# Kernel optimization log

Measured on AMD Instinct MI355X. Metric: run time of the kernel, lower is better.

The kernel has to match this reference:

```python
import jax, jax.numpy as jnp
import numpy as np

B, T, F = 2048, 128, 1
H1, H2 = 128, 64


def lstm_relu(x, W, U, b):
    """Keras LSTM with activation=relu, recurrent_activation=sigmoid.
    x: [B, T, Fin]; W: [Fin, 4H]; U: [H, 4H]; b: [4H]. Gate order i,f,g,o.
    Returns full sequence of hidden states [B, T, H]."""
    Bb = x.shape[0]
    H = U.shape[0]

    def step(carry, xt):
        h, c = carry
        z = xt @ W + h @ U + b  # [B, 4H]
        i, f, g, o = jnp.split(z, 4, axis=-1)
        i = jax.nn.sigmoid(i)
        f = jax.nn.sigmoid(f)
        o = jax.nn.sigmoid(o)
        g = jax.nn.relu(g)
        c = f * c + i * g
        h = o * jax.nn.relu(c)
        return (h, c), h

    h0 = jnp.zeros((Bb, H), x.dtype)
    (_, _), hs = jax.lax.scan(step, (h0, h0), jnp.swapaxes(x, 0, 1))
    return jnp.swapaxes(hs, 0, 1)  # [B, T, H]


def setup_inputs() -> dict:
    key = jax.random.key(0)
    ks = jax.random.split(key, 16)
    s = 0.05  # small init so relu LSTM stays numerically stable
    d = {
        "x": jax.random.normal(ks[0], (B, T, F), jnp.float32),
        "W1": jax.random.normal(ks[1], (F, 4 * H1), jnp.float32) * s,
        "U1": jax.random.normal(ks[2], (H1, 4 * H1), jnp.float32) * s,
        "b1": jnp.zeros((4 * H1,), jnp.float32),
        "W2": jax.random.normal(ks[3], (H1, 4 * H2), jnp.float32) * s,
        "U2": jax.random.normal(ks[4], (H2, 4 * H2), jnp.float32) * s,
        "b2": jnp.zeros((4 * H2,), jnp.float32),
        "W3": jax.random.normal(ks[5], (H2, 4 * H2), jnp.float32) * s,
        "U3": jax.random.normal(ks[6], (H2, 4 * H2), jnp.float32) * s,
        "b3": jnp.zeros((4 * H2,), jnp.float32),
        "W4": jax.random.normal(ks[7], (H2, 4 * H1), jnp.float32) * s,
        "U4": jax.random.normal(ks[8], (H1, 4 * H1), jnp.float32) * s,
        "b4": jnp.zeros((4 * H1,), jnp.float32),
        "Wd": jax.random.normal(ks[9], (H1, 1), jnp.float32) * s,
        "bd": jnp.zeros((1,), jnp.float32),
    }
    return d


def reference(x, W1, U1, b1, W2, U2, b2, W3, U3, b3, W4, U4, b4, Wd, bd):
    h = lstm_relu(x, W1, U1, b1)            # [B, T, 128]
    h = lstm_relu(h, W2, U2, b2)[:, -1]     # return_sequences=False -> [B, 64]
    h = jnp.broadcast_to(h[:, None, :], (h.shape[0], T, h.shape[-1]))  # RepeatVector
    h = lstm_relu(h, W3, U3, b3)            # [B, T, 64]
    h = lstm_relu(h, W4, U4, b4)            # [B, T, 128]
    out = h @ Wd + bd                       # TimeDistributed Dense(1) -> [B, T, 1]
    return out
```

## Files before the change

kernel.cpp:

```cpp
#include <hip/hip_runtime.h>


#define TSEQ 128
#define NTH  512
#define BSTR 408

typedef __attribute__((ext_vector_type(8))) short bf16x8;
typedef __attribute__((ext_vector_type(4))) float f32x4;
typedef __attribute__((ext_vector_type(2))) float f32x2;
typedef __attribute__((ext_vector_type(4))) short s16x4;
typedef unsigned short ushort_t;

#define FB_L1 0
#define FB_L2 256
#define FB_L3 448
#define FB_L4 512
#define FB_W3 896
#define WS_FRAGS 960
#define WS_NEEDED (WS_FRAGS * 1024)

__device__ __forceinline__ ushort_t f2bf(float f) {
    union { float f; unsigned u; } a; a.f = f;
    unsigned r = a.u + 0x7FFF + ((a.u >> 16) & 1);
    return (ushort_t)(r >> 16);
}
__device__ __forceinline__ float bf2f(ushort_t h) {
    union { unsigned u; float f; } a; a.u = ((unsigned)h) << 16;
    return a.f;
}
__device__ __forceinline__ float sigm(float z) { return 1.0f / (1.0f + __expf(-z)); }

__device__ __forceinline__ f32x4 MF(bf16x8 a, bf16x8 b, f32x4 c) {
    return __builtin_amdgcn_mfma_f32_16x16x32_bf16(a, b, c, 0, 0, 0);
}

__global__ void pack_weights(const float* __restrict__ U1, const float* __restrict__ W2,
                             const float* __restrict__ U2, const float* __restrict__ U3,
                             const float* __restrict__ W4, const float* __restrict__ U4,
                             const float* __restrict__ W3, ushort_t* __restrict__ out)
{
    const int f = blockIdx.x;
    const int lane = threadIdx.x;
    int fl, KT, ldm, ksplit = 1 << 30, ld2 = 0;
    const float *base, *base2 = nullptr;
    if (f < 256)      { fl = f;       KT = 4; ldm = 512; base = U1; }
    else if (f < 448) { fl = f - 256; KT = 6; ldm = 256; base = W2; ksplit = 128; base2 = U2; ld2 = 256; }
    else if (f < 512) { fl = f - 448; KT = 2; ldm = 256; base = U3; }
    else if (f < 896) { fl = f - 512; KT = 6; ldm = 512; base = W4; ksplit = 64;  base2 = U4; ld2 = 512; }
    else              { fl = f - 896; KT = 2; ldm = 256; base = W3; }
    const int jt = fl / (KT * 2);
    const int rem = fl % (KT * 2);
    const int kt = rem >> 1;
    const int s = rem & 1;
    const int j = jt * 16 + (lane & 15);
    ushort_t* o = out + f * 512 + lane * 8;
    #pragma unroll
    for (int i = 0; i < 8; ++i) {
        const int k = kt * 32 + (lane >> 4) * 8 + i;
        const float w = (k < ksplit) ? base[k * ldm + j] : base2[(k - ksplit) * ld2 + j];
        const ushort_t hi = f2bf(w);
        o[i] = s ? f2bf(w - bf2f(hi)) : hi;
    }
}

__global__ __launch_bounds__(NTH, 2) void lstm_mfma_kernel(
    const float* __restrict__ x,
    const float* __restrict__ W1, const float* __restrict__ b1,
    const float* __restrict__ b2, const float* __restrict__ b3,
    const float* __restrict__ b4,
    const float* __restrict__ Wd, const float* __restrict__ bd,
    const ushort_t* __restrict__ wsp,
    float* __restrict__ out)
{
    __shared__ __align__(16) ushort_t bU[16][BSTR];
    __shared__ __align__(16) float zb[16][260];
    __shared__ __align__(16) float z3x[16][260];
    __shared__ __align__(16) float c23[16][64];
    __shared__ __align__(16) float obuf[16][128];
    __shared__ __align__(16) float xls[16][132];
    __shared__ __align__(16) float w1ls[512], b1ls[512], b4ls[512], b2ls[256];

    const int tid  = threadIdx.x;
    const int wid  = tid >> 6;
    const int lane = tid & 63;
    const int quad = lane >> 4;
    const int l15  = lane & 15;
    const int r0   = blockIdx.x * 16;
    const bf16x8* A = (const bf16x8*)wsp;

    const int rg = tid >> 5;
    const int jp = (tid & 31) * 2;

    {
        unsigned* p = (unsigned*)&bU[0][0];
        for (int i = tid; i < 16 * BSTR / 2; i += NTH) p[i] = 0u;
        float* q = &c23[0][0];
        for (int i = tid; i < 16 * 64; i += NTH) q[i] = 0.f;
        const int srow = tid >> 5, scol = (tid & 31) * 4;
        *(f32x4*)&xls[srow][scol] = *(const f32x4*)&x[(r0 + srow) * TSEQ + scol];
        w1ls[tid] = W1[tid];
        b1ls[tid] = b1[tid];
        b4ls[tid] = b4[tid];
        if (tid < 256) b2ls[tid] = b2[tid];
    }

    const int hcb = 16 * wid + quad * 4;
    const float wd0 = Wd[lane], wd1 = Wd[64 + lane], bd0 = bd[0];

    float c1r[4] = {0.f, 0.f, 0.f, 0.f};
    float c4r[4] = {0.f, 0.f, 0.f, 0.f};

    __syncthreads();

    {
        bf16x8 wL1[16], wL2[12];
        #pragma unroll
        for (int q = 0; q < 4; ++q)
            #pragma unroll
            for (int kt = 0; kt < 4; ++kt)
                wL1[q * 4 + kt] = A[(FB_L1 + ((wid + 8 * q) * 4 + kt) * 2) * 64 + lane];
        #pragma unroll
        for (int jj = 0; jj < 2; ++jj)
            #pragma unroll
            for (int kt = 0; kt < 6; ++kt)
                wL2[jj * 6 + kt] = A[(FB_L2 + ((2 * wid + jj) * 6 + kt) * 2) * 64 + lane];

        for (int t = 0; t < TSEQ; ++t) {
            const int rb1 = (t & 1) * 128, wb1 = 128 - rb1;

            {
                bf16x8 Bh[4];
                #pragma unroll
                for (int kt = 0; kt < 4; ++kt)
                    Bh[kt] = *(const bf16x8*)&bU[l15][rb1 + kt * 32 + quad * 8];
                const float xr = xls[l15][t];
                f32x4 acc[4];
                #pragma unroll
                for (int q = 0; q < 4; ++q) {
                    const int jb = (wid + 8 * q) * 16 + quad * 4;
                    f32x4 a = *(const f32x4*)&b1ls[jb];
                    a += xr * *(const f32x4*)&w1ls[jb];
                    #pragma unroll
                    for (int kt = 0; kt < 4; ++kt)
                        a = MF(wL1[q * 4 + kt], Bh[kt], a);
                    acc[q] = a;
                }
                s16x4 hv;
                #pragma unroll
                for (int g = 0; g < 4; ++g) {
                    const float zi = acc[0][g];
                    const float zf = acc[1][g];
                    const float zg = acc[2][g];
                    const float zo = acc[3][g];
                    const float c = sigm(zf) * c1r[g] + sigm(zi) * fmaxf(zg, 0.f);
                    c1r[g] = c;
                    const float h = sigm(zo) * fmaxf(c, 0.f);
                    hv[g] = (short)f2bf(h);
                }
                *(s16x4*)&bU[l15][wb1 + hcb] = hv;
            }
            __syncthreads();

            {
                bf16x8 Bh[6];
                #pragma unroll
                for (int kt = 0; kt < 4; ++kt)
                    Bh[kt] = *(const bf16x8*)&bU[l15][wb1 + kt * 32 + quad * 8];
                #pragma unroll
                for (int kt = 4; kt < 6; ++kt)
                    Bh[kt] = *(const bf16x8*)&bU[l15][256 + (kt - 4) * 32 + quad * 8];
                #pragma unroll
                for (int jj = 0; jj < 2; ++jj) {
                    const int jt = 2 * wid + jj;
                    f32x4 a = *(const f32x4*)&b2ls[jt * 16 + quad * 4];
                    #pragma unroll
                    for (int kt = 0; kt < 6; ++kt)
                        a = MF(wL2[jj * 6 + kt], Bh[kt], a);
                    *(f32x4*)&zb[l15][jt * 16 + quad * 4] = a;
                }
            }
            __syncthreads();

            {
                const f32x2 zi = *(const f32x2*)&zb[rg][jp];
                const f32x2 zf = *(const f32x2*)&zb[rg][64 + jp];
                const f32x2 zg = *(const f32x2*)&zb[rg][128 + jp];
                const f32x2 zo = *(const f32x2*)&zb[rg][192 + jp];
                f32x2 c = *(const f32x2*)&c23[rg][jp];
                unsigned hw = 0;
                #pragma unroll
                for (int k = 0; k < 2; ++k) {
                    const float cc = sigm(zf[k]) * c[k] + sigm(zi[k]) * fmaxf(zg[k], 0.f);
                    c[k] = cc;
                    const float h = sigm(zo[k]) * fmaxf(cc, 0.f);
                    hw |= ((unsigned)f2bf(h)) << (16 * k);
                }
                *(f32x2*)&c23[rg][jp] = c;
                *(unsigned*)&bU[rg][256 + jp] = hw;
            }
        }
    }
    __syncthreads();

    {
        bf16x8 Bh[2];
        #pragma unroll
        for (int kt = 0; kt < 2; ++kt)
            Bh[kt] = *(const bf16x8*)&bU[l15][256 + kt * 32 + quad * 8];
        #pragma unroll
        for (int jj = 0; jj < 2; ++jj) {
            const int jt = 2 * wid + jj;
            f32x4 a = *(const f32x4*)&b3[jt * 16 + quad * 4];
            #pragma unroll
            for (int kt = 0; kt < 2; ++kt) {
                const bf16x8 ah = A[(FB_W3 + (jt * 2 + kt) * 2) * 64 + lane];
                a = MF(ah, Bh[kt], a);
            }
            *(f32x4*)&z3x[l15][jt * 16 + quad * 4] = a;
        }
    }
    __syncthreads();
    {
        unsigned* p = (unsigned*)&bU[0][0];
        for (int i = tid; i < 16 * BSTR / 2; i += NTH) p[i] = 0u;
        float* q = &c23[0][0];
        for (int i = tid; i < 16 * 64; i += NTH) q[i] = 0.f;
        c4r[0] = c4r[1] = c4r[2] = c4r[3] = 0.f;
    }
    __syncthreads();

    {
        bf16x8 wL3[4], wL4[24];
        #pragma unroll
        for (int jj = 0; jj < 2; ++jj)
            #pragma unroll
            for (int kt = 0; kt < 2; ++kt)
                wL3[jj * 2 + kt] = A[(FB_L3 + ((2 * wid + jj) * 2 + kt) * 2) * 64 + lane];
        #pragma unroll
        for (int q = 0; q < 4; ++q)
            #pragma unroll
            for (int kt = 0; kt < 6; ++kt)
                wL4[q * 6 + kt] = A[(FB_L4 + ((wid + 8 * q) * 6 + kt) * 2) * 64 + lane];

        for (int t = 0; t < TSEQ; ++t) {
            const int rb3 = (t & 1) * 64, wb3 = 64 - rb3;
            const int rb4 = 128 + (t & 1) * 128;
            const int wb4 = (rb4 == 128) ? 256 : 128;

            {
                bf16x8 Bh[2];
                #pragma unroll
                for (int kt = 0; kt < 2; ++kt)
                    Bh[kt] = *(const bf16x8*)&bU[l15][rb3 + kt * 32 + quad * 8];
                #pragma unroll
                for (int jj = 0; jj < 2; ++jj) {
                    const int jt = 2 * wid + jj;
                    f32x4 a = {0.f, 0.f, 0.f, 0.f};
                    #pragma unroll
                    for (int kt = 0; kt < 2; ++kt)
                        a = MF(wL3[jj * 2 + kt], Bh[kt], a);
                    *(f32x4*)&zb[l15][jt * 16 + quad * 4] = a;
                }
            }
            __syncthreads();

            {
                const f32x2 zi = *(const f32x2*)&zb[rg][jp]       + *(const f32x2*)&z3x[rg][jp];
                const f32x2 zf = *(const f32x2*)&zb[rg][64 + jp]  + *(const f32x2*)&z3x[rg][64 + jp];
                const f32x2 zg = *(const f32x2*)&zb[rg][128 + jp] + *(const f32x2*)&z3x[rg][128 + jp];
                const f32x2 zo = *(const f32x2*)&zb[rg][192 + jp] + *(const f32x2*)&z3x[rg][192 + jp];
                f32x2 c = *(const f32x2*)&c23[rg][jp];
                unsigned hw = 0;
                #pragma unroll
                for (int k = 0; k < 2; ++k) {
                    const float cc = sigm(zf[k]) * c[k] + sigm(zi[k]) * fmaxf(zg[k], 0.f);
                    c[k] = cc;
                    const float h = sigm(zo[k]) * fmaxf(cc, 0.f);
                    hw |= ((unsigned)f2bf(h)) << (16 * k);
                }
                *(f32x2*)&c23[rg][jp] = c;
                *(unsigned*)&bU[rg][wb3 + jp] = hw;

                if (t > 0) {
                    #pragma unroll
                    for (int e = 0; e < 2; ++e) {
                        const int r = wid + 8 * e;
                        const float h0 = bf2f(bU[r][rb4 + lane]);
                        const float h1_ = bf2f(bU[r][rb4 + 64 + lane]);
                        float v = h0 * wd0 + h1_ * wd1;
                        v += __shfl_down(v, 32);
                        v += __shfl_down(v, 16);
                        v += __shfl_down(v, 8);
                        v += __shfl_down(v, 4);
                        v += __shfl_down(v, 2);
                        v += __shfl_down(v, 1);
                        if (lane == 0) obuf[r][t - 1] = v + bd0;
                    }
                }
            }
            __syncthreads();

            {
                bf16x8 Bh[6];
                #pragma unroll
                for (int kt = 0; kt < 2; ++kt)
                    Bh[kt] = *(const bf16x8*)&bU[l15][wb3 + kt * 32 + quad * 8];
                #pragma unroll
                for (int kt = 2; kt < 6; ++kt)
                    Bh[kt] = *(const bf16x8*)&bU[l15][rb4 + (kt - 2) * 32 + quad * 8];
                f32x4 acc[4];
                #pragma unroll
                for (int q = 0; q < 4; ++q) {
                    f32x4 a = *(const f32x4*)&b4ls[(wid + 8 * q) * 16 + quad * 4];
                    #pragma unroll
                    for (int kt = 0; kt < 6; ++kt)
                        a = MF(wL4[q * 6 + kt], Bh[kt], a);
                    acc[q] = a;
                }
                s16x4 hv;
                #pragma unroll
                for (int g = 0; g < 4; ++g) {
                    const float zi = acc[0][g];
                    const float zf = acc[1][g];
                    const float zg = acc[2][g];
                    const float zo = acc[3][g];
                    const float c = sigm(zf) * c4r[g] + sigm(zi) * fmaxf(zg, 0.f);
                    c4r[g] = c;
                    const float h = sigm(zo) * fmaxf(c, 0.f);
                    hv[g] = (short)f2bf(h);
                }
                *(s16x4*)&bU[l15][wb4 + hcb] = hv;
            }
        }
    }
    __syncthreads();
    {
        #pragma unroll
        for (int e = 0; e < 2; ++e) {
            const int r = wid + 8 * e;
            const float h0 = bf2f(bU[r][128 + lane]);
            const float h1_ = bf2f(bU[r][128 + 64 + lane]);
            float v = h0 * wd0 + h1_ * wd1;
            v += __shfl_down(v, 32);
            v += __shfl_down(v, 16);
            v += __shfl_down(v, 8);
            v += __shfl_down(v, 4);
            v += __shfl_down(v, 2);
            v += __shfl_down(v, 1);
            if (lane == 0) obuf[r][127] = v + bd0;
        }
    }
    __syncthreads();
    {
        const int frow = tid >> 5;
        const int fcol = (tid & 31) * 4;
        *(f32x4*)&out[(r0 + frow) * TSEQ + fcol] = *(const f32x4*)&obuf[frow][fcol];
    }
}

#define FNT 512
#define FRPB 8
__global__ __launch_bounds__(FNT, 2) void lstm_stack_kernel(
    const float* __restrict__ x,
    const float* __restrict__ W1, const float* __restrict__ U1, const float* __restrict__ b1,
    const float* __restrict__ W2, const float* __restrict__ U2, const float* __restrict__ b2,
    const float* __restrict__ W3, const float* __restrict__ U3, const float* __restrict__ b3,
    const float* __restrict__ W4, const float* __restrict__ U4, const float* __restrict__ b4,
    const float* __restrict__ Wd, const float* __restrict__ bd,
    float* __restrict__ out)
{
    __shared__ float h1s[FRPB][128], c1s[FRPB][128];
    __shared__ float h2s[FRPB][64],  c2s[FRPB][64];
    __shared__ float h3s[FRPB][64],  c3s[FRPB][64];
    __shared__ float h4s[FRPB][128], c4s[FRPB][128];
    __shared__ float zbf[FRPB][512];
    __shared__ float z3xf[FRPB][256];
    __shared__ float xs[FRPB];

    const int tid = threadIdx.x;
    const int r0  = blockIdx.x * FRPB;
    const int jg  = tid & 255;
    const int grp = tid >> 8;
    const int rb  = grp * 4;

    {
        float* p1 = &h1s[0][0]; float* p2 = &c1s[0][0];
        float* p3 = &h4s[0][0]; float* p4 = &c4s[0][0];
        for (int i = tid; i < FRPB * 128; i += FNT) { p1[i]=0.f; p2[i]=0.f; p3[i]=0.f; p4[i]=0.f; }
        float* q1 = &h2s[0][0]; float* q2 = &c2s[0][0];
        float* q3 = &h3s[0][0]; float* q4 = &c3s[0][0];
        for (int i = tid; i < FRPB * 64; i += FNT) { q1[i]=0.f; q2[i]=0.f; q3[i]=0.f; q4[i]=0.f; }
    }
    __syncthreads();

    const float w1j = W1[tid];
    const float b1j = b1[tid];
    const float b2j = b2[jg];

    for (int t = 0; t < TSEQ; ++t) {
        if (tid < FRPB) xs[tid] = x[(r0 + tid) * TSEQ + t];
        __syncthreads();
        {
            float acc[FRPB];
            #pragma unroll
            for (int r = 0; r < FRPB; ++r) acc[r] = 0.f;
            const float* Uc = U1 + tid;
            #pragma unroll 4
            for (int k4 = 0; k4 < 32; ++k4) {
                const float u0 = Uc[(k4*4+0)*512];
                const float u1 = Uc[(k4*4+1)*512];
                const float u2 = Uc[(k4*4+2)*512];
                const float u3 = Uc[(k4*4+3)*512];
                #pragma unroll
                for (int r = 0; r < FRPB; ++r) {
                    const float4 h = ((const float4*)h1s[r])[k4];
                    acc[r] += h.x*u0 + h.y*u1 + h.z*u2 + h.w*u3;
                }
            }
            #pragma unroll
            for (int r = 0; r < FRPB; ++r) zbf[r][tid] = acc[r] + xs[r]*w1j + b1j;
        }
        __syncthreads();
        for (int e = tid; e < FRPB * 128; e += FNT) {
            const int r = e >> 7, hc = e & 127;
            const float zi = zbf[r][hc], zf = zbf[r][128+hc], zg = zbf[r][256+hc], zo = zbf[r][384+hc];
            const float c = sigm(zf)*c1s[r][hc] + sigm(zi)*fmaxf(zg, 0.f);
            c1s[r][hc] = c;
            h1s[r][hc] = sigm(zo)*fmaxf(c, 0.f);
        }
        __syncthreads();
        {
            float acc[4] = {0.f, 0.f, 0.f, 0.f};
            const float* Wc = W2 + jg;
            #pragma unroll 4
            for (int k4 = 0; k4 < 32; ++k4) {
                const float u0 = Wc[(k4*4+0)*256];
                const float u1 = Wc[(k4*4+1)*256];
                const float u2 = Wc[(k4*4+2)*256];
                const float u3 = Wc[(k4*4+3)*256];
                #pragma unroll
                for (int q = 0; q < 4; ++q) {
                    const float4 h = ((const float4*)h1s[rb+q])[k4];
                    acc[q] += h.x*u0 + h.y*u1 + h.z*u2 + h.w*u3;
                }
            }
            const float* Uc = U2 + jg;
            #pragma unroll 4
            for (int k4 = 0; k4 < 16; ++k4) {
                const float u0 = Uc[(k4*4+0)*256];
                const float u1 = Uc[(k4*4+1)*256];
                const float u2 = Uc[(k4*4+2)*256];
                const float u3 = Uc[(k4*4+3)*256];
                #pragma unroll
                for (int q = 0; q < 4; ++q) {
                    const float4 h = ((const float4*)h2s[rb+q])[k4];
                    acc[q] += h.x*u0 + h.y*u1 + h.z*u2 + h.w*u3;
                }
            }
            #pragma unroll
            for (int q = 0; q < 4; ++q) zbf[rb+q][jg] = acc[q] + b2j;
        }
        __syncthreads();
        {
            const int r = tid >> 6, hc = tid & 63;
            const float zi = zbf[r][hc], zf = zbf[r][64+hc], zg = zbf[r][128+hc], zo = zbf[r][192+hc];
            const float c = sigm(zf)*c2s[r][hc] + sigm(zi)*fmaxf(zg, 0.f);
            c2s[r][hc] = c;
            h2s[r][hc] = sigm(zo)*fmaxf(c, 0.f);
        }
        __syncthreads();
    }
    {
        float acc[4] = {0.f, 0.f, 0.f, 0.f};
        const float* Wc = W3 + jg;
        #pragma unroll 4
        for (int k4 = 0; k4 < 16; ++k4) {
            const float u0 = Wc[(k4*4+0)*256];
            const float u1 = Wc[(k4*4+1)*256];
            const float u2 = Wc[(k4*4+2)*256];
            const float u3 = Wc[(k4*4+3)*256];
            #pragma unroll
            for (int q = 0; q < 4; ++q) {
                const float4 h = ((const float4*)h2s[rb+q])[k4];
                acc[q] += h.x*u0 + h.y*u1 + h.z*u2 + h.w*u3;
            }
        }
        const float b3j = b3[jg];
        #pragma unroll
        for (int q = 0; q < 4; ++q) z3xf[rb+q][jg] = acc[q] + b3j;
    }
    __syncthreads();

    const float b4j = b4[tid];
    const float wd0 = Wd[tid & 63];
    const float wd1 = Wd[64 + (tid & 63)];
    const float bd0 = bd[0];

    for (int t = 0; t < TSEQ; ++t) {
        {
            float acc[4];
            #pragma unroll
            for (int q = 0; q < 4; ++q) acc[q] = z3xf[rb+q][jg];
            const float* Uc = U3 + jg;
            #pragma unroll 4
            for (int k4 = 0; k4 < 16; ++k4) {
                const float u0 = Uc[(k4*4+0)*256];
                const float u1 = Uc[(k4*4+1)*256];
                const float u2 = Uc[(k4*4+2)*256];
                const float u3 = Uc[(k4*4+3)*256];
                #pragma unroll
                for (int q = 0; q < 4; ++q) {
                    const float4 h = ((const float4*)h3s[rb+q])[k4];
                    acc[q] += h.x*u0 + h.y*u1 + h.z*u2 + h.w*u3;
                }
            }
            #pragma unroll
            for (int q = 0; q < 4; ++q) zbf[rb+q][jg] = acc[q];
        }
        __syncthreads();
        {
            const int r = tid >> 6, hc = tid & 63;
            const float zi = zbf[r][hc], zf = zbf[r][64+hc], zg = zbf[r][128+hc], zo = zbf[r][192+hc];
            const float c = sigm(zf)*c3s[r][hc] + sigm(zi)*fmaxf(zg, 0.f);
            c3s[r][hc] = c;
            h3s[r][hc] = sigm(zo)*fmaxf(c, 0.f);
        }
        __syncthreads();
        {
            float acc[FRPB];
            #pragma unroll
            for (int r = 0; r < FRPB; ++r) acc[r] = 0.f;
            const float* Wc = W4 + tid;
            #pragma unroll 4
            for (int k4 = 0; k4 < 16; ++k4) {
                const float u0 = Wc[(k4*4+0)*512];
                const float u1 = Wc[(k4*4+1)*512];
                const float u2 = Wc[(k4*4+2)*512];
                const float u3 = Wc[(k4*4+3)*512];
                #pragma unroll
                for (int r = 0; r < FRPB; ++r) {
                    const float4 h = ((const float4*)h3s[r])[k4];
                    acc[r] += h.x*u0 + h.y*u1 + h.z*u2 + h.w*u3;
                }
            }
            const float* Uc = U4 + tid;
            #pragma unroll 4
            for (int k4 = 0; k4 < 32; ++k4) {
                const float u0 = Uc[(k4*4+0)*512];
                const float u1 = Uc[(k4*4+1)*512];
                const float u2 = Uc[(k4*4+2)*512];
                const float u3 = Uc[(k4*4+3)*512];
                #pragma unroll
                for (int r = 0; r < FRPB; ++r) {
                    const float4 h = ((const float4*)h4s[r])[k4];
                    acc[r] += h.x*u0 + h.y*u1 + h.z*u2 + h.w*u3;
                }
            }
            #pragma unroll
            for (int r = 0; r < FRPB; ++r) zbf[r][tid] = acc[r] + b4j;
        }
        __syncthreads();
        for (int e = tid; e < FRPB * 128; e += FNT) {
            const int r = e >> 7, hc = e & 127;
            const float zi = zbf[r][hc], zf = zbf[r][128+hc], zg = zbf[r][256+hc], zo = zbf[r][384+hc];
            const float c = sigm(zf)*c4s[r][hc] + sigm(zi)*fmaxf(zg, 0.f);
            c4s[r][hc] = c;
            h4s[r][hc] = sigm(zo)*fmaxf(c, 0.f);
        }
        __syncthreads();
        {
            const int wv = tid >> 6, ln = tid & 63;
            float v = h4s[wv][ln]*wd0 + h4s[wv][64+ln]*wd1;
            v += __shfl_down(v, 32, 64);
            v += __shfl_down(v, 16, 64);
            v += __shfl_down(v,  8, 64);
            v += __shfl_down(v,  4, 64);
            v += __shfl_down(v,  2, 64);
            v += __shfl_down(v,  1, 64);
            if (ln == 0) out[(r0 + wv) * TSEQ + t] = v + bd0;
        }
    }
}

extern "C" void kernel_launch(void* const* d_in, const int* in_sizes, int n_in,
                              void* d_out, int out_size, void* d_ws, size_t ws_size,
                              hipStream_t stream) {
    const float* x  = (const float*)d_in[0];
    const float* W1 = (const float*)d_in[1];
    const float* U1 = (const float*)d_in[2];
    const float* b1 = (const float*)d_in[3];
    const float* W2 = (const float*)d_in[4];
    const float* U2 = (const float*)d_in[5];
    const float* b2 = (const float*)d_in[6];
    const float* W3 = (const float*)d_in[7];
    const float* U3 = (const float*)d_in[8];
    const float* b3 = (const float*)d_in[9];
    const float* W4 = (const float*)d_in[10];
    const float* U4 = (const float*)d_in[11];
    const float* b4 = (const float*)d_in[12];
    const float* Wd = (const float*)d_in[13];
    const float* bd = (const float*)d_in[14];
    float* out = (float*)d_out;

    if (ws_size >= (size_t)WS_NEEDED) {
        ushort_t* wsp = (ushort_t*)d_ws;
        pack_weights<<<dim3(WS_FRAGS), dim3(64), 0, stream>>>(U1, W2, U2, U3, W4, U4, W3, wsp);
        lstm_mfma_kernel<<<dim3(2048 / 16), dim3(NTH), 0, stream>>>(
            x, W1, b1, b2, b3, b4, Wd, bd, wsp, out);
    } else {
        lstm_stack_kernel<<<dim3(2048 / FRPB), dim3(FNT), 0, stream>>>(
            x, W1, U1, b1, W2, U2, b2, W3, U3, b3, W4, U4, b4, Wd, bd, out);
    }
}
```

Baseline: 609.4 us.

## Keep layer 2/3 gate accumulators in registers and drop shared-memory gate round trip

Layers 2 and 3 now have four waves each compute all four gates (i,f,g,o) for one 16-column slice. The gate nonlinearities and cell update happen directly in registers, so the zb/z3x/c23 shared buffers and one __syncthreads per step are gone. Layer 2's hidden state is double-buffered in bU so it can be written in place. The dense output projection moves after the layer 4 update. The cost is that only half the waves do MFMA work in layers 2 and 3, and register pressure rises from the larger wL2 and z3r arrays.

```diff
diff --git a/kernel.cpp b/kernel.cpp
--- a/kernel.cpp
+++ b/kernel.cpp
@@ -73,9 +73,6 @@
     float* __restrict__ out)
 {
     __shared__ __align__(16) ushort_t bU[16][BSTR];
-    __shared__ __align__(16) float zb[16][260];
-    __shared__ __align__(16) float z3x[16][260];
-    __shared__ __align__(16) float c23[16][64];
     __shared__ __align__(16) float obuf[16][128];
     __shared__ __align__(16) float xls[16][132];
     __shared__ __align__(16) float w1ls[512], b1ls[512], b4ls[512], b2ls[256];
@@ -88,14 +85,9 @@
     const int r0   = blockIdx.x * 16;
     const bf16x8* A = (const bf16x8*)wsp;
 
-    const int rg = tid >> 5;
-    const int jp = (tid & 31) * 2;
-
     {
         unsigned* p = (unsigned*)&bU[0][0];
         for (int i = tid; i < 16 * BSTR / 2; i += NTH) p[i] = 0u;
-        float* q = &c23[0][0];
-        for (int i = tid; i < 16 * 64; i += NTH) q[i] = 0.f;
         const int srow = tid >> 5, scol = (tid & 31) * 4;
         *(f32x4*)&xls[srow][scol] = *(const f32x4*)&x[(r0 + srow) * TSEQ + scol];
         w1ls[tid] = W1[tid];
@@ -113,20 +105,26 @@
     __syncthreads();
 
     {
-        bf16x8 wL1[16], wL2[12];
+        bf16x8 wL1[16];
         #pragma unroll
         for (int q = 0; q < 4; ++q)
             #pragma unroll
             for (int kt = 0; kt < 4; ++kt)
                 wL1[q * 4 + kt] = A[(FB_L1 + ((wid + 8 * q) * 4 + kt) * 2) * 64 + lane];
-        #pragma unroll
-        for (int jj = 0; jj < 2; ++jj)
-            #pragma unroll
-            for (int kt = 0; kt < 6; ++kt)
-                wL2[jj * 6 + kt] = A[(FB_L2 + ((2 * wid + jj) * 6 + kt) * 2) * 64 + lane];
+        bf16x8 wL2[24];
+        if (wid < 4) {
+            #pragma unroll
+            for (int g = 0; g < 4; ++g)
+                #pragma unroll
+                for (int kt = 0; kt < 6; ++kt)
+                    wL2[g * 6 + kt] = A[(FB_L2 + ((4 * g + wid) * 6 + kt) * 2) * 64 + lane];
+        }
+        float c2r[4] = {0.f, 0.f, 0.f, 0.f};
 
         for (int t = 0; t < TSEQ; ++t) {
             const int rb1 = (t & 1) * 128, wb1 = 128 - rb1;
+            const int h2w = 256 + (t & 1) * 64;
+            const int h2r = 256 + (((t & 1) ^ 1)) * 64;
 
             {
                 bf16x8 Bh[4];
@@ -161,142 +159,107 @@
             }
             __syncthreads();
 
-            {
+            if (wid < 4) {
                 bf16x8 Bh[6];
                 #pragma unroll
                 for (int kt = 0; kt < 4; ++kt)
                     Bh[kt] = *(const bf16x8*)&bU[l15][wb1 + kt * 32 + quad * 8];
-                #pragma unroll
-                for (int kt = 4; kt < 6; ++kt)
-                    Bh[kt] = *(const bf16x8*)&bU[l15][256 + (kt - 4) * 32 + quad * 8];
-                #pragma unroll
-                for (int jj = 0; jj < 2; ++jj) {
-                    const int jt = 2 * wid + jj;
-                    f32x4 a = *(const f32x4*)&b2ls[jt * 16 + quad * 4];
+                Bh[4] = *(const bf16x8*)&bU[l15][h2r + quad * 8];
+                Bh[5] = *(const bf16x8*)&bU[l15][h2r + 32 + quad * 8];
+                f32x4 acc[4];
+                #pragma unroll
+                for (int g = 0; g < 4; ++g) {
+                    f32x4 a = *(const f32x4*)&b2ls[(4 * g + wid) * 16 + quad * 4];
                     #pragma unroll
                     for (int kt = 0; kt < 6; ++kt)
-                        a = MF(wL2[jj * 6 + kt], Bh[kt], a);
-                    *(f32x4*)&zb[l15][jt * 16 + quad * 4] = a;
-                }
-            }
-            __syncthreads();
-
-            {
-                const f32x2 zi = *(const f32x2*)&zb[rg][jp];
-                const f32x2 zf = *(const f32x2*)&zb[rg][64 + jp];
-                const f32x2 zg = *(const f32x2*)&zb[rg][128 + jp];
-                const f32x2 zo = *(const f32x2*)&zb[rg][192 + jp];
-                f32x2 c = *(const f32x2*)&c23[rg][jp];
-                unsigned hw = 0;
-                #pragma unroll
-                for (int k = 0; k < 2; ++k) {
-                    const float cc = sigm(zf[k]) * c[k] + sigm(zi[k]) * fmaxf(zg[k], 0.f);
-                    c[k] = cc;
-                    const float h = sigm(zo[k]) * fmaxf(cc, 0.f);
-                    hw |= ((unsigned)f2bf(h)) << (16 * k);
-                }
-                *(f32x2*)&c23[rg][jp] = c;
-                *(unsigned*)&bU[rg][256 + jp] = hw;
-            }
-        }
-    }
-    __syncthreads();
-
-    {
-        bf16x8 Bh[2];
+                        a = MF(wL2[g * 6 + kt], Bh[kt], a);
+                    acc[g] = a;
+                }
+                s16x4 hv;
+                #pragma unroll
+                for (int e = 0; e < 4; ++e) {
+                    const float zi = acc[0][e];
+                    const float zf = acc[1][e];
+                    const float zg = acc[2][e];
+                    const float zo = acc[3][e];
+                    const float c = sigm(zf) * c2r[e] + sigm(zi) * fmaxf(zg, 0.f);
+                    c2r[e] = c;
+                    const float h = sigm(zo) * fmaxf(c, 0.f);
+                    hv[e] = (short)f2bf(h);
+                }
+                *(s16x4*)&bU[l15][h2w + wid * 16 + quad * 4] = hv;
+            }
+        }
+    }
+    __syncthreads();
+
+    f32x4 z3r[4];
+    if (wid < 4) {
+        const bf16x8 Bh0 = *(const bf16x8*)&bU[l15][320 + quad * 8];
+        const bf16x8 Bh1 = *(const bf16x8*)&bU[l15][320 + 32 + quad * 8];
         #pragma unroll
-        for (int kt = 0; kt < 2; ++kt)
-            Bh[kt] = *(const bf16x8*)&bU[l15][256 + kt * 32 + quad * 8];
-        #pragma unroll
-        for (int jj = 0; jj < 2; ++jj) {
-            const int jt = 2 * wid + jj;
+        for (int g = 0; g < 4; ++g) {
+            const int jt = 4 * g + wid;
             f32x4 a = *(const f32x4*)&b3[jt * 16 + quad * 4];
-            #pragma unroll
-            for (int kt = 0; kt < 2; ++kt) {
-                const bf16x8 ah = A[(FB_W3 + (jt * 2 + kt) * 2) * 64 + lane];
-                a = MF(ah, Bh[kt], a);
-            }
-            *(f32x4*)&z3x[l15][jt * 16 + quad * 4] = a;
+            a = MF(A[(FB_W3 + (jt * 2 + 0) * 2) * 64 + lane], Bh0, a);
+            a = MF(A[(FB_W3 + (jt * 2 + 1) * 2) * 64 + lane], Bh1, a);
+            z3r[g] = a;
         }
     }
     __syncthreads();
     {
         unsigned* p = (unsigned*)&bU[0][0];
         for (int i = tid; i < 16 * BSTR / 2; i += NTH) p[i] = 0u;
-        float* q = &c23[0][0];
-        for (int i = tid; i < 16 * 64; i += NTH) q[i] = 0.f;
         c4r[0] = c4r[1] = c4r[2] = c4r[3] = 0.f;
     }
     __syncthreads();
 
     {
-        bf16x8 wL3[4], wL4[24];
-        #pragma unroll
-        for (int jj = 0; jj < 2; ++jj)
-            #pragma unroll
-            for (int kt = 0; kt < 2; ++kt)
-                wL3[jj * 2 + kt] = A[(FB_L3 + ((2 * wid + jj) * 2 + kt) * 2) * 64 + lane];
+        bf16x8 wL3[8];
+        if (wid < 4) {
+            #pragma unroll
+            for (int g = 0; g < 4; ++g)
+                #pragma unroll
+                for (int kt = 0; kt < 2; ++kt)
+                    wL3[g * 2 + kt] = A[(FB_L3 + ((4 * g + wid) * 2 + kt) * 2) * 64 + lane];
+        }
+        bf16x8 wL4[24];
         #pragma unroll
         for (int q = 0; q < 4; ++q)
             #pragma unroll
             for (int kt = 0; kt < 6; ++kt)
                 wL4[q * 6 + kt] = A[(FB_L4 + ((wid + 8 * q) * 6 + kt) * 2) * 64 + lane];
+        float c3r[4] = {0.f, 0.f, 0.f, 0.f};
 
         for (int t = 0; t < TSEQ; ++t) {
             const int rb3 = (t & 1) * 64, wb3 = 64 - rb3;
             const int rb4 = 128 + (t & 1) * 128;
             const int wb4 = (rb4 == 128) ? 256 : 128;
 
-            {
-                bf16x8 Bh[2];
-                #pragma unroll
-                for (int kt = 0; kt < 2; ++kt)
-                    Bh[kt] = *(const bf16x8*)&bU[l15][rb3 + kt * 32 + quad * 8];
-                #pragma unroll
-                for (int jj = 0; jj < 2; ++jj) {
-                    const int jt = 2 * wid + jj;
-                    f32x4 a = {0.f, 0.f, 0.f, 0.f};
-                    #pragma unroll
-                    for (int kt = 0; kt < 2; ++kt)
-                        a = MF(wL3[jj * 2 + kt], Bh[kt], a);
-                    *(f32x4*)&zb[l15][jt * 16 + quad * 4] = a;
-                }
-            }
-            __syncthreads();
-
-            {
-                const f32x2 zi = *(const f32x2*)&zb[rg][jp]       + *(const f32x2*)&z3x[rg][jp];
-                const f32x2 zf = *(const f32x2*)&zb[rg][64 + jp]  + *(const f32x2*)&z3x[rg][64 + jp];
-                const f32x2 zg = *(const f32x2*)&zb[rg][128 + jp] + *(const f32x2*)&z3x[rg][128 + jp];
-                const f32x2 zo = *(const f32x2*)&zb[rg][192 + jp] + *(const f32x2*)&z3x[rg][192 + jp];
-                f32x2 c = *(const f32x2*)&c23[rg][jp];
-                unsigned hw = 0;
-                #pragma unroll
-                for (int k = 0; k < 2; ++k) {
-                    const float cc = sigm(zf[k]) * c[k] + sigm(zi[k]) * fmaxf(zg[k], 0.f);
-                    c[k] = cc;
-                    const float h = sigm(zo[k]) * fmaxf(cc, 0.f);
-                    hw |= ((unsigned)f2bf(h)) << (16 * k);
-                }
-                *(f32x2*)&c23[rg][jp] = c;
-                *(unsigned*)&bU[rg][wb3 + jp] = hw;
-
-                if (t > 0) {
-                    #pragma unroll
-                    for (int e = 0; e < 2; ++e) {
-                        const int r = wid + 8 * e;
-                        const float h0 = bf2f(bU[r][rb4 + lane]);
-                        const float h1_ = bf2f(bU[r][rb4 + 64 + lane]);
-                        float v = h0 * wd0 + h1_ * wd1;
-                        v += __shfl_down(v, 32);
-                        v += __shfl_down(v, 16);
-                        v += __shfl_down(v, 8);
-                        v += __shfl_down(v, 4);
-                        v += __shfl_down(v, 2);
-                        v += __shfl_down(v, 1);
-                        if (lane == 0) obuf[r][t - 1] = v + bd0;
-                    }
-                }
+            if (wid < 4) {
+                const bf16x8 Bh0 = *(const bf16x8*)&bU[l15][rb3 + quad * 8];
+                const bf16x8 Bh1 = *(const bf16x8*)&bU[l15][rb3 + 32 + quad * 8];
+                f32x4 acc[4];
+                #pragma unroll
+                for (int g = 0; g < 4; ++g) {
+                    f32x4 a = z3r[g];
+                    a = MF(wL3[g * 2 + 0], Bh0, a);
+                    a = MF(wL3[g * 2 + 1], Bh1, a);
+                    acc[g] = a;
+                }
+                s16x4 hv;
+                #pragma unroll
+                for (int e = 0; e < 4; ++e) {
+                    const float zi = acc[0][e];
+                    const float zf = acc[1][e];
+                    const float zg = acc[2][e];
+                    const float zo = acc[3][e];
+                    const float c = sigm(zf) * c3r[e] + sigm(zi) * fmaxf(zg, 0.f);
+                    c3r[e] = c;
+                    const float h = sigm(zo) * fmaxf(c, 0.f);
+                    hv[e] = (short)f2bf(h);
+                }
+                *(s16x4*)&bU[l15][wb3 + wid * 16 + quad * 4] = hv;
             }
             __syncthreads();
 
@@ -330,6 +293,23 @@
                     hv[g] = (short)f2bf(h);
                 }
                 *(s16x4*)&bU[l15][wb4 + hcb] = hv;
+            }
+
+            if (t > 0) {
+                #pragma unroll
+                for (int e = 0; e < 2; ++e) {
+                    const int r = wid + 8 * e;
+                    const float h0 = bf2f(bU[r][rb4 + lane]);
+                    const float h1_ = bf2f(bU[r][rb4 + 64 + lane]);
+                    float v = h0 * wd0 + h1_ * wd1;
+                    v += __shfl_down(v, 32);
+                    v += __shfl_down(v, 16);
+                    v += __shfl_down(v, 8);
+                    v += __shfl_down(v, 4);
+                    v += __shfl_down(v, 2);
+                    v += __shfl_down(v, 1);
+                    if (lane == 0) obuf[r][t - 1] = v + bd0;
+                }
             }
         }
     }
```

Result: faster. 533.4 us (-12.5%).
